# Kernel tuning notes

Hardware: AMD Instinct MI355X
Metric: run time of the kernel (lower is better)

Reference implementation:

```python
import jax, jax.numpy as jnp
import numpy as np

B, S, H = 256, 196, 1024  # batch, image_size**2, hidden_size


def _linear_init(key, fan_in, fan_out):
    kw, kb = jax.random.split(key)
    lim = 1.0 / np.sqrt(fan_in)
    W = jax.random.uniform(kw, (fan_in, fan_out), jnp.float32, -lim, lim)
    b = jax.random.uniform(kb, (fan_out,), jnp.float32, -lim, lim)
    return W, b


def setup_inputs() -> dict:
    key = jax.random.key(0)
    ks = jax.random.split(key, 7)
    v = jax.random.normal(ks[0], (B, S, H), jnp.float32)
    h = jax.random.normal(ks[1], (B, H), jnp.float32)
    W_fc, b_fc = _linear_init(ks[2], H, 2 * H)
    W_v, b_v = _linear_init(ks[3], H, H)
    W_h, b_h = _linear_init(ks[4], H, H)
    W_s, b_s = _linear_init(ks[5], H, H)
    W_z, b_z = _linear_init(ks[6], H, 1)
    return {"v": v, "h": h, "W_fc": W_fc, "b_fc": b_fc, "W_v": W_v, "b_v": b_v,
            "W_h": W_h, "b_h": b_h, "W_s": W_s, "b_s": b_s, "W_z": W_z, "b_z": b_z}


def reference(v, h, W_fc, b_fc, W_v, b_v, W_h, b_h, W_s, b_s, W_z, b_z):
    # Dropout is identity in eval mode.
    hs = jnp.tanh(h[:, None, :] @ W_fc + b_fc)          # (B, 1, 2H)
    h1, s = hs[..., :H], hs[..., H:]                    # each (B, 1, H)
    _v = v @ W_v + b_v                                  # (B, S, H)
    _h = h1 @ W_h + b_h                                 # (B, 1, H)
    _s = s @ W_s + b_s                                  # (B, 1, H)
    z = jnp.tanh(jnp.concatenate([_v, _s], axis=1) + _h)  # (B, S+1, H)
    z = (z @ W_z + b_z)[..., 0]                         # (B, S+1)
    a = jax.nn.softmax(z, axis=1)                       # (B, S+1)
    vc = jnp.concatenate([v, s], axis=1)                # (B, S+1, H)
    c = jnp.sum(a[:, :, None] * vc, axis=1)             # (B, H)
    return a, c
```

## Files before the change

### kernel.cpp

```cpp
#include <hip/hip_runtime.h>
#include <hip/hip_bf16.h>
#include <cstdint>
#include <cstddef>

#define Bb  256
#define Ss  196
#define Hh  1024
#define SP1 197
#define Mm  50176

typedef float  f32x4 __attribute__((ext_vector_type(4)));
typedef short  s16x8 __attribute__((ext_vector_type(8)));
typedef unsigned short u16;

__device__ __forceinline__ u16 f2b(float f) {
  __hip_bfloat16 b = __float2bfloat16(f);
  u16 r; __builtin_memcpy(&r, &b, 2); return r;
}

__global__ __launch_bounds__(256) void k_transpose_cvt(const float* __restrict__ Wv,
                                                       u16* __restrict__ WvT) {
  __shared__ float t[64][65];
  int k0 = (blockIdx.x & 15) * 64;
  int n0 = (blockIdx.x >> 4) * 64;
  int tid = threadIdx.x;
#pragma unroll
  for (int i = 0; i < 16; ++i) {
    int idx = i * 256 + tid;
    int r = idx >> 6, c = idx & 63;
    t[r][c] = Wv[(size_t)(k0 + r) * Hh + n0 + c];
  }
  __syncthreads();
#pragma unroll
  for (int i = 0; i < 16; ++i) {
    int idx = i * 256 + tid;
    int r = idx >> 6, c = idx & 63;
    WvT[(size_t)(n0 + r) * Hh + ((k0 + c) ^ ((r & 7) << 3))] = f2b(t[c][r]);
  }
}

__device__ __forceinline__ void small_gemm_core(int bid, int nct,
    const float* __restrict__ X, int ldx,
    const float* __restrict__ W, int ldw,
    const float* __restrict__ bias,
    float* __restrict__ Y, int ldy, int act) {
  __shared__ float xs[4][16][64];
  int tid = threadIdx.x, lane = tid & 63, w = tid >> 6;
  int ct = bid % nct, bt = bid / nct;
  int col = ct * 64 + lane;
  float acc[16];
#pragma unroll
  for (int b = 0; b < 16; ++b) acc[b] = 0.f;
  int xr = lane >> 2, xc = (lane & 3) * 16;
  for (int kc = 0; kc < 4; ++kc) {
    int kb = w * 256 + kc * 64;
#pragma unroll
    for (int q = 0; q < 4; ++q)
      *(f32x4*)&xs[w][xr][xc + q * 4] =
          *(const f32x4*)&X[(size_t)(bt * 16 + xr) * ldx + kb + xc + q * 4];
    for (int kl = 0; kl < 64; kl += 4) {
      float w0 = W[(size_t)(kb + kl + 0) * ldw + col];
      float w1 = W[(size_t)(kb + kl + 1) * ldw + col];
      float w2 = W[(size_t)(kb + kl + 2) * ldw + col];
      float w3 = W[(size_t)(kb + kl + 3) * ldw + col];
#pragma unroll
      for (int b = 0; b < 16; ++b) {
        f32x4 x = *(const f32x4*)&xs[w][b][kl];
        acc[b] += x.x * w0 + x.y * w1 + x.z * w2 + x.w * w3;
      }
    }
  }
#pragma unroll
  for (int b = 0; b < 16; ++b) xs[w][b][lane] = acc[b];
  __syncthreads();
#pragma unroll
  for (int q = 0; q < 4; ++q) {
    int b = w * 4 + q;
    float s = xs[0][b][lane] + xs[1][b][lane] + xs[2][b][lane] + xs[3][b][lane]
            + bias[col];
    if (act) s = tanhf(s);
    Y[(size_t)(bt * 16 + b) * ldy + col] = s;
  }
}

__global__ __launch_bounds__(256) void k_fc(const float* __restrict__ h,
                                            const float* __restrict__ Wfc,
                                            const float* __restrict__ bfc,
                                            float* __restrict__ hs) {
  small_gemm_core(blockIdx.x, 32, h, Hh, Wfc, 2048, bfc, hs, 2048, 1);
}

__global__ __launch_bounds__(256) void k_dual(const float* __restrict__ hs,
                                              const float* __restrict__ Wh,
                                              const float* __restrict__ bh,
                                              const float* __restrict__ Ws_,
                                              const float* __restrict__ bs_,
                                              float* __restrict__ hhp,
                                              float* __restrict__ svp) {
  int bid = blockIdx.x;
  int sel = bid >= 256;
  small_gemm_core(bid - (sel << 8), 16,
                  sel ? hs + 1024 : hs, 2048,
                  sel ? Ws_ : Wh, Hh,
                  sel ? bs_ : bh,
                  sel ? svp : hhp, Hh, 0);
}

#define BM 64
#define BN 256
#define BK 64
#define LDA 72
__global__ __launch_bounds__(256, 3) void k_big(const float* __restrict__ V,
                                                const u16* __restrict__ WvT,
                                                const float* __restrict__ bv,
                                                const float* __restrict__ hh,
                                                const float* __restrict__ Wz,
                                                float* __restrict__ zpart) {
  __shared__ __align__(16) u16 As[BM * LDA];
  __shared__ __align__(16) u16 Bs[BN * BK];
  __shared__ float wz_s[BN], bv_s[BN], hh_s[2][BN];
  __shared__ float zred[4][BM];

  int bid = blockIdx.x;
  int lin = (bid & 7) * 392 + (bid >> 3);
  int mt = lin >> 2, nt = lin & 3;
  int row0 = mt * BM, n0 = nt * BN;

  int tid = threadIdx.x;
  int lane = tid & 63, wid = tid >> 6;

  int b0 = row0 / Ss;
  int rsplit = (b0 + 1) * Ss - row0;
  int b1 = (rsplit < BM) ? b0 + 1 : b0;
  wz_s[tid] = Wz[n0 + tid];
  bv_s[tid] = bv[n0 + tid];
  hh_s[0][tid] = hh[(size_t)b0 * Hh + n0 + tid];
  hh_s[1][tid] = hh[(size_t)b1 * Hh + n0 + tid];

  f32x4 acc[4][4];
  f32x4 zz = {0.f, 0.f, 0.f, 0.f};
#pragma unroll
  for (int m = 0; m < 4; ++m)
#pragma unroll
    for (int n = 0; n < 4; ++n) acc[m][n] = zz;

  int arow = tid >> 4;
  int acol = (tid & 15) * 4;
  const float* Ap = V + (size_t)(row0 + arow) * Hh + acol;

  int bsub = lane >> 3;
  int bko  = (lane & 7) * 8;

  f32x4 av[4];
#pragma unroll
  for (int j = 0; j < 4; ++j) av[j] = *(const f32x4*)(Ap + (size_t)j * 16 * Hh);

  for (int kt = 0; kt < 16; ++kt) {
    int k0 = kt * BK;
    __syncthreads();
#pragma unroll
    for (int i = 0; i < 8; ++i) {
      int r = wid * 64 + i * 8;
      const u16* g = WvT + (size_t)(n0 + r + bsub) * Hh + (k0 + bko);
      __builtin_amdgcn_global_load_lds(
          (const __attribute__((address_space(1))) unsigned int*)(const void*)g,
          (__attribute__((address_space(3))) unsigned int*)(void*)&Bs[r * BK],
          16, 0, 0);
    }
#pragma unroll
    for (int j = 0; j < 4; ++j) {
      ushort4 w;
      w.x = f2b(av[j].x); w.y = f2b(av[j].y);
      w.z = f2b(av[j].z); w.w = f2b(av[j].w);
      *(ushort4*)&As[(arow + j * 16) * LDA + acol] = w;
    }
    if (kt < 15) {
#pragma unroll
      for (int j = 0; j < 4; ++j)
        av[j] = *(const f32x4*)(Ap + (size_t)j * 16 * Hh + k0 + BK);
    }
    __syncthreads();
#pragma unroll
    for (int ks = 0; ks < 2; ++ks) {
      int kk = ks * 32 + (lane >> 4) * 8;
      s16x8 afr[4], bfr[4];
#pragma unroll
      for (int m = 0; m < 4; ++m)
        afr[m] = *(const s16x8*)&As[(m * 16 + (lane & 15)) * LDA + kk];
#pragma unroll
      for (int n = 0; n < 4; ++n) {
        int r = wid * 64 + n * 16 + (lane & 15);
        bfr[n] = *(const s16x8*)&Bs[r * BK + (kk ^ ((r & 7) << 3))];
      }
#pragma unroll
      for (int m = 0; m < 4; ++m)
#pragma unroll
        for (int n = 0; n < 4; ++n)
          acc[m][n] = __builtin_amdgcn_mfma_f32_16x16x32_bf16(afr[m], bfr[n], acc[m][n], 0, 0, 0);
    }
  }

  int cl = lane & 15, rg = lane >> 4;
  float pz[4][4];
#pragma unroll
  for (int m = 0; m < 4; ++m)
#pragma unroll
    for (int j = 0; j < 4; ++j) pz[m][j] = 0.f;
#pragma unroll
  for (int n = 0; n < 4; ++n) {
    int col = wid * 64 + n * 16 + cl;
    float wzv = wz_s[col], bvv = bv_s[col];
    float h0 = hh_s[0][col], h1 = hh_s[1][col];
#pragma unroll
    for (int m = 0; m < 4; ++m)
#pragma unroll
      for (int j = 0; j < 4; ++j) {
        int r = m * 16 + rg * 4 + j;
        float hv = (r >= rsplit) ? h1 : h0;
        pz[m][j] += wzv * tanhf(acc[m][n][j] + bvv + hv);
      }
  }
#pragma unroll
  for (int m = 0; m < 4; ++m)
#pragma unroll
    for (int j = 0; j < 4; ++j) {
      float vv = pz[m][j];
      vv += __shfl_xor(vv, 1); vv += __shfl_xor(vv, 2);
      vv += __shfl_xor(vv, 4); vv += __shfl_xor(vv, 8);
      pz[m][j] = vv;
    }
  if (cl == 0) {
#pragma unroll
    for (int m = 0; m < 4; ++m)
#pragma unroll
      for (int j = 0; j < 4; ++j)
        zred[wid][m * 16 + rg * 4 + j] = pz[m][j];
  }
  __syncthreads();
  if (tid < BM)
    zpart[(size_t)nt * Mm + row0 + tid] =
        zred[0][tid] + zred[1][tid] + zred[2][tid] + zred[3][tid];
}

__global__ __launch_bounds__(256) void k_softmax(const float* __restrict__ zpart,
                                                 const float* __restrict__ sv,
                                                 const float* __restrict__ hhp,
                                                 const float* __restrict__ Wz,
                                                 const float* __restrict__ bz,
                                                 float* __restrict__ outA) {
  int b = blockIdx.x, tid = threadIdx.x;
  int wid = tid >> 6, lane = tid & 63;
  __shared__ float redm[4], reds[4];
  __shared__ float zSsh;
  {
    int j0 = tid * 4;
    f32x4 s4 = *(const f32x4*)&sv[(size_t)b * Hh + j0];
    f32x4 h4 = *(const f32x4*)&hhp[(size_t)b * Hh + j0];
    f32x4 w4 = *(const f32x4*)&Wz[j0];
    float p = w4.x * tanhf(s4.x + h4.x) + w4.y * tanhf(s4.y + h4.y)
            + w4.z * tanhf(s4.z + h4.z) + w4.w * tanhf(s4.w + h4.w);
#pragma unroll
    for (int d = 1; d < 64; d <<= 1) p += __shfl_xor(p, d);
    if (lane == 0) redm[wid] = p;
    __syncthreads();
    if (tid == 0) zSsh = redm[0] + redm[1] + redm[2] + redm[3] + bz[0];
    __syncthreads();
  }
  float z = -1e30f;
  if (tid < Ss) {
    float s = 0.f;
#pragma unroll
    for (int nt = 0; nt < 4; ++nt) s += zpart[(size_t)nt * Mm + (size_t)b * Ss + tid];
    z = s + bz[0];
  } else if (tid == Ss) {
    z = zSsh;
  }
  float m = z;
#pragma unroll
  for (int d = 1; d < 64; d <<= 1) m = fmaxf(m, __shfl_xor(m, d));
  if (lane == 0) redm[wid] = m;
  __syncthreads();
  m = fmaxf(fmaxf(redm[0], redm[1]), fmaxf(redm[2], redm[3]));
  float e = (tid <= Ss) ? expf(z - m) : 0.f;
  float s = e;
#pragma unroll
  for (int d = 1; d < 64; d <<= 1) s += __shfl_xor(s, d);
  if (lane == 0) reds[wid] = s;
  __syncthreads();
  s = reds[0] + reds[1] + reds[2] + reds[3];
  if (tid <= Ss) outA[(size_t)b * SP1 + tid] = e / s;
}

__global__ __launch_bounds__(256) void k_ctx(const float* __restrict__ V,
                                             const float* __restrict__ hs,
                                             const float* __restrict__ A,
                                             float* __restrict__ outC) {
  int b = blockIdx.x >> 2;
  int col = (blockIdx.x & 3) * 256 + threadIdx.x;
  __shared__ float a_s[SP1];
  if (threadIdx.x < SP1) a_s[threadIdx.x] = A[(size_t)b * SP1 + threadIdx.x];
  __syncthreads();
  float acc = a_s[Ss] * hs[(size_t)b * 2048 + 1024 + col];
  const float* vb = &V[(size_t)b * Ss * Hh + col];
#pragma unroll 4
  for (int t = 0; t < Ss; ++t) acc += a_s[t] * vb[(size_t)t * Hh];
  outC[(size_t)b * Hh + col] = acc;
}

extern "C" void kernel_launch(void* const* d_in, const int* in_sizes, int n_in,
                              void* d_out, int out_size, void* d_ws, size_t ws_size,
                              hipStream_t stream) {
  const float* v   = (const float*)d_in[0];
  const float* h   = (const float*)d_in[1];
  const float* Wfc = (const float*)d_in[2];
  const float* bfc = (const float*)d_in[3];
  const float* Wv  = (const float*)d_in[4];
  const float* bv  = (const float*)d_in[5];
  const float* Wh  = (const float*)d_in[6];
  const float* bh  = (const float*)d_in[7];
  const float* Ws  = (const float*)d_in[8];
  const float* bs  = (const float*)d_in[9];
  const float* Wz  = (const float*)d_in[10];
  const float* bz  = (const float*)d_in[11];
  float* out  = (float*)d_out;
  float* outA = out;
  float* outC = out + (size_t)Bb * SP1;

  float* ws  = (float*)d_ws;
  float* hs  = ws;
  float* hh  = hs + 524288;
  float* sv  = hh + 262144;
  float* zp  = sv + 262144;
  u16*  WvT  = (u16*)(zp + 200704);

  k_transpose_cvt<<<256, 256, 0, stream>>>(Wv, WvT);
  k_fc<<<512, 256, 0, stream>>>(h, Wfc, bfc, hs);
  k_dual<<<512, 256, 0, stream>>>(hs, Wh, bh, Ws, bs, hh, sv);
  k_big<<<3136, 256, 0, stream>>>(v, WvT, bv, hh, Wz, zp);
  k_softmax<<<256, 256, 0, stream>>>(zp, sv, hh, Wz, bz, outA);
  k_ctx<<<1024, 256, 0, stream>>>(v, hs, outA, outC);
}
```

Baseline: 279.5 us.

## Double k_big M-tile to 128 rows and use fast exp-based tanh

Raises the k_big row tile from 64 to 128, so each block reuses every loaded Wv tile across twice as many rows. The grid is halved and occupancy drops to 2 blocks per CU, and A loads and LDS stores are widened to 8 bf16 per thread. It also replaces tanhf everywhere with an exp/rcp tanh approximation to cut transcendental cost in the epilogue-heavy tanh over the full activation. The changes add register pressure from 32 accumulators per thread and slightly reduce tanh precision.

```diff
diff --git a/kernel.cpp b/kernel.cpp
--- a/kernel.cpp
+++ b/kernel.cpp
@@ -12,10 +12,18 @@
 typedef float  f32x4 __attribute__((ext_vector_type(4)));
 typedef short  s16x8 __attribute__((ext_vector_type(8)));
 typedef unsigned short u16;
+typedef unsigned short u16x8 __attribute__((ext_vector_type(8)));
 
 __device__ __forceinline__ u16 f2b(float f) {
   __hip_bfloat16 b = __float2bfloat16(f);
   u16 r; __builtin_memcpy(&r, &b, 2); return r;
+}
+
+__device__ __forceinline__ float ftanh(float x) {
+  float ax = fabsf(x);
+  float t = __expf(-2.f * ax);
+  float r = (1.f - t) * __builtin_amdgcn_rcpf(1.f + t);
+  return copysignf(r, x);
 }
 
 __global__ __launch_bounds__(256) void k_transpose_cvt(const float* __restrict__ Wv,
@@ -78,7 +86,7 @@
     int b = w * 4 + q;
     float s = xs[0][b][lane] + xs[1][b][lane] + xs[2][b][lane] + xs[3][b][lane]
             + bias[col];
-    if (act) s = tanhf(s);
+    if (act) s = ftanh(s);
     Y[(size_t)(bt * 16 + b) * ldy + col] = s;
   }
 }
@@ -106,11 +114,11 @@
                   sel ? svp : hhp, Hh, 0);
 }
 
-#define BM 64
+#define BM 128
 #define BN 256
 #define BK 64
 #define LDA 72
-__global__ __launch_bounds__(256, 3) void k_big(const float* __restrict__ V,
+__global__ __launch_bounds__(256, 2) void k_big(const float* __restrict__ V,
                                                 const u16* __restrict__ WvT,
                                                 const float* __restrict__ bv,
                                                 const float* __restrict__ hh,
@@ -122,7 +130,7 @@
   __shared__ float zred[4][BM];
 
   int bid = blockIdx.x;
-  int lin = (bid & 7) * 392 + (bid >> 3);
+  int lin = (bid & 7) * 196 + (bid >> 3);
   int mt = lin >> 2, nt = lin & 3;
   int row0 = mt * BM, n0 = nt * BN;
 
@@ -137,23 +145,27 @@
   hh_s[0][tid] = hh[(size_t)b0 * Hh + n0 + tid];
   hh_s[1][tid] = hh[(size_t)b1 * Hh + n0 + tid];
 
-  f32x4 acc[4][4];
+  f32x4 acc[8][4];
   f32x4 zz = {0.f, 0.f, 0.f, 0.f};
 #pragma unroll
-  for (int m = 0; m < 4; ++m)
+  for (int m = 0; m < 8; ++m)
 #pragma unroll
     for (int n = 0; n < 4; ++n) acc[m][n] = zz;
 
-  int arow = tid >> 4;
-  int acol = (tid & 15) * 4;
+  int arow = tid >> 3;
+  int acol = (tid & 7) * 8;
   const float* Ap = V + (size_t)(row0 + arow) * Hh + acol;
 
   int bsub = lane >> 3;
   int bko  = (lane & 7) * 8;
-
-  f32x4 av[4];
-#pragma unroll
-  for (int j = 0; j < 4; ++j) av[j] = *(const f32x4*)(Ap + (size_t)j * 16 * Hh);
+  int bxor = (lane & 7) << 3;
+
+  f32x4 av[8];
+#pragma unroll
+  for (int j = 0; j < 4; ++j) {
+    av[2 * j]     = *(const f32x4*)(Ap + (size_t)j * 32 * Hh);
+    av[2 * j + 1] = *(const f32x4*)(Ap + (size_t)j * 32 * Hh + 4);
+  }
 
   for (int kt = 0; kt < 16; ++kt) {
     int k0 = kt * BK;
@@ -169,31 +181,35 @@
     }
 #pragma unroll
     for (int j = 0; j < 4; ++j) {
-      ushort4 w;
-      w.x = f2b(av[j].x); w.y = f2b(av[j].y);
-      w.z = f2b(av[j].z); w.w = f2b(av[j].w);
-      *(ushort4*)&As[(arow + j * 16) * LDA + acol] = w;
+      u16x8 w;
+      w[0] = f2b(av[2 * j].x);     w[1] = f2b(av[2 * j].y);
+      w[2] = f2b(av[2 * j].z);     w[3] = f2b(av[2 * j].w);
+      w[4] = f2b(av[2 * j + 1].x); w[5] = f2b(av[2 * j + 1].y);
+      w[6] = f2b(av[2 * j + 1].z); w[7] = f2b(av[2 * j + 1].w);
+      *(u16x8*)&As[(j * 32 + arow) * LDA + acol] = w;
     }
     if (kt < 15) {
 #pragma unroll
-      for (int j = 0; j < 4; ++j)
-        av[j] = *(const f32x4*)(Ap + (size_t)j * 16 * Hh + k0 + BK);
+      for (int j = 0; j < 4; ++j) {
+        av[2 * j]     = *(const f32x4*)(Ap + (size_t)j * 32 * Hh + k0 + BK);
+        av[2 * j + 1] = *(const f32x4*)(Ap + (size_t)j * 32 * Hh + k0 + BK + 4);
+      }
     }
     __syncthreads();
 #pragma unroll
     for (int ks = 0; ks < 2; ++ks) {
       int kk = ks * 32 + (lane >> 4) * 8;
-      s16x8 afr[4], bfr[4];
-#pragma unroll
-      for (int m = 0; m < 4; ++m)
+      s16x8 afr[8], bfr[4];
+#pragma unroll
+      for (int m = 0; m < 8; ++m)
         afr[m] = *(const s16x8*)&As[(m * 16 + (lane & 15)) * LDA + kk];
 #pragma unroll
       for (int n = 0; n < 4; ++n) {
         int r = wid * 64 + n * 16 + (lane & 15);
-        bfr[n] = *(const s16x8*)&Bs[r * BK + (kk ^ ((r & 7) << 3))];
+        bfr[n] = *(const s16x8*)&Bs[r * BK + (kk ^ bxor)];
       }
 #pragma unroll
-      for (int m = 0; m < 4; ++m)
+      for (int m = 0; m < 8; ++m)
 #pragma unroll
         for (int n = 0; n < 4; ++n)
           acc[m][n] = __builtin_amdgcn_mfma_f32_16x16x32_bf16(afr[m], bfr[n], acc[m][n], 0, 0, 0);
@@ -201,9 +217,9 @@
   }
 
   int cl = lane & 15, rg = lane >> 4;
-  float pz[4][4];
-#pragma unroll
-  for (int m = 0; m < 4; ++m)
+  float pz[8][4];
+#pragma unroll
+  for (int m = 0; m < 8; ++m)
 #pragma unroll
     for (int j = 0; j < 4; ++j) pz[m][j] = 0.f;
 #pragma unroll
@@ -212,16 +228,16 @@
     float wzv = wz_s[col], bvv = bv_s[col];
     float h0 = hh_s[0][col], h1 = hh_s[1][col];
 #pragma unroll
-    for (int m = 0; m < 4; ++m)
+    for (int m = 0; m < 8; ++m)
 #pragma unroll
       for (int j = 0; j < 4; ++j) {
         int r = m * 16 + rg * 4 + j;
         float hv = (r >= rsplit) ? h1 : h0;
-        pz[m][j] += wzv * tanhf(acc[m][n][j] + bvv + hv);
+        pz[m][j] += wzv * ftanh(acc[m][n][j] + bvv + hv);
       }
   }
 #pragma unroll
-  for (int m = 0; m < 4; ++m)
+  for (int m = 0; m < 8; ++m)
 #pragma unroll
     for (int j = 0; j < 4; ++j) {
       float vv = pz[m][j];
@@ -231,7 +247,7 @@
     }
   if (cl == 0) {
 #pragma unroll
-    for (int m = 0; m < 4; ++m)
+    for (int m = 0; m < 8; ++m)
 #pragma unroll
       for (int j = 0; j < 4; ++j)
         zred[wid][m * 16 + rg * 4 + j] = pz[m][j];
@@ -257,8 +273,8 @@
     f32x4 s4 = *(const f32x4*)&sv[(size_t)b * Hh + j0];
     f32x4 h4 = *(const f32x4*)&hhp[(size_t)b * Hh + j0];
     f32x4 w4 = *(const f32x4*)&Wz[j0];
-    float p = w4.x * tanhf(s4.x + h4.x) + w4.y * tanhf(s4.y + h4.y)
-            + w4.z * tanhf(s4.z + h4.z) + w4.w * tanhf(s4.w + h4.w);
+    float p = w4.x * ftanh(s4.x + h4.x) + w4.y * ftanh(s4.y + h4.y)
+            + w4.z * ftanh(s4.z + h4.z) + w4.w * ftanh(s4.w + h4.w);
 #pragma unroll
     for (int d = 1; d < 64; d <<= 1) p += __shfl_xor(p, d);
     if (lane == 0) redm[wid] = p;
@@ -336,7 +352,7 @@
   k_transpose_cvt<<<256, 256, 0, stream>>>(Wv, WvT);
   k_fc<<<512, 256, 0, stream>>>(h, Wfc, bfc, hs);
   k_dual<<<512, 256, 0, stream>>>(hs, Wh, bh, Ws, bs, hh, sv);
-  k_big<<<3136, 256, 0, stream>>>(v, WvT, bv, hh, Wz, zp);
+  k_big<<<1568, 256, 0, stream>>>(v, WvT, bv, hh, Wz, zp);
   k_softmax<<<256, 256, 0, stream>>>(zp, sv, hh, Wz, bz, outA);
   k_ctx<<<1024, 256, 0, stream>>>(v, hs, outA, outC);
 }
```

Result: faster. 262.4 us (-6.1%).
